# Kernel tuning notes

Measured on AMD Instinct MI355X. Metric: run time of the kernel, lower is better.

## Reference

```python
import jax, jax.numpy as jnp
import numpy as np

N_NODES = 50000
N_EDGES = 800000
IN_FEAT = 128
HID = 64
HEADS = 4
OUT = 40
NEG_SLOPE = 0.2


def _p(key, shape, scale=0.05):
    return jax.random.normal(key, shape, dtype=jnp.float32) * scale


def setup_inputs() -> dict:
    key = jax.random.key(0)
    ks = jax.random.split(key, 20)
    HW = HID * HEADS  # 256
    inp = {
        "x": jax.random.normal(ks[0], (N_NODES, IN_FEAT), dtype=jnp.float32),
        "edge_index": jax.random.randint(ks[1], (2, N_EDGES), 0, N_NODES, dtype=jnp.int64),
        # GATConv 1: in=128 -> heads=4, C=64
        "W1": _p(ks[2], (IN_FEAT, HW)), "as1": _p(ks[3], (HEADS, HID)), "ad1": _p(ks[4], (HEADS, HID)), "b1": jnp.zeros((HW,), jnp.float32),
        # GATConv 2: in=256
        "W2": _p(ks[5], (HW, HW)), "as2": _p(ks[6], (HEADS, HID)), "ad2": _p(ks[7], (HEADS, HID)), "b2": jnp.zeros((HW,), jnp.float32),
        # GATConv 3: in=256
        "W3": _p(ks[8], (HW, HW)), "as3": _p(ks[9], (HEADS, HID)), "ad3": _p(ks[10], (HEADS, HID)), "b3": jnp.zeros((HW,), jnp.float32),
        # MLP head: Linear(256,256) + Linear(256,40)
        "Wm1": _p(ks[11], (HW, HW)), "bm1": jnp.zeros((HW,), jnp.float32),
        "Wm2": _p(ks[12], (HW, OUT)), "bm2": jnp.zeros((OUT,), jnp.float32),
    }
    return inp


def gat_conv(x, src, dst, W, a_src, a_dst, bias, num_nodes):
    """PyG GATConv: concat=True, add_self_loops=True, leaky_relu(0.2)."""
    H, C = a_src.shape
    h = (x @ W).reshape(num_nodes, H, C)            # [N,H,C]
    # per-node attention logits (computed once, gathered per edge)
    src_logit = jnp.einsum('nhc,hc->nh', h, a_src)  # [N,H]
    dst_logit = jnp.einsum('nhc,hc->nh', h, a_dst)  # [N,H]
    # add self loops
    loop = jnp.arange(num_nodes, dtype=src.dtype)
    s = jnp.concatenate([src, loop])
    d = jnp.concatenate([dst, loop])
    alpha = jax.nn.leaky_relu(src_logit[s] + dst_logit[d], NEG_SLOPE)  # [E,H]
    # segment softmax over incoming edges of each destination node
    amax = jax.ops.segment_max(alpha, d, num_segments=num_nodes)
    e = jnp.exp(alpha - amax[d])
    denom = jax.ops.segment_sum(e, d, num_segments=num_nodes)
    coef = e / denom[d]                              # [E,H]
    msg = h[s] * coef[:, :, None]                    # [E,H,C] gather+weight
    out = jax.ops.segment_sum(msg, d, num_segments=num_nodes)  # [N,H,C]
    return out.reshape(num_nodes, H * C) + bias


def reference(x, edge_index, W1, as1, ad1, b1, W2, as2, ad2, b2, W3, as3, ad3, b3, Wm1, bm1, Wm2, bm2):
    src, dst = edge_index[0], edge_index[1]
    n = x.shape[0]
    h = jax.nn.relu(gat_conv(x, src, dst, W1, as1, ad1, b1, n))
    h = jax.nn.relu(gat_conv(h, src, dst, W2, as2, ad2, b2, n))
    h = jax.nn.relu(gat_conv(h, src, dst, W3, as3, ad3, b3, n))
    h = jax.nn.relu(h @ Wm1 + bm1)
    return h @ Wm2 + bm2
```

## Files before the change

kernel.cpp:

```cpp
#include <hip/hip_runtime.h>


constexpr int NN = 50000;
constexpr int NE = 800000;
constexpr int NN_PAD = 50176;
constexpr int CAP = 48;

typedef _Float16 f16x8 __attribute__((ext_vector_type(8)));
typedef _Float16 f16x4 __attribute__((ext_vector_type(4)));
typedef float    f32x4 __attribute__((ext_vector_type(4)));

__device__ __forceinline__ void cp16(void* lds, const void* g)
{
    __builtin_amdgcn_global_load_lds(
        (const __attribute__((address_space(1))) uint32_t*)g,
        (__attribute__((address_space(3))) uint32_t*)lds, 16, 0, 0);
}

__global__ __launch_bounds__(256)
void convert_all_kernel(const float* __restrict__ W1, const float* __restrict__ W2,
                        const float* __restrict__ W3, const float* __restrict__ Wm1,
                        const float* __restrict__ Wm2,
                        _Float16* B1h, _Float16* B1l, _Float16* B2h, _Float16* B2l,
                        _Float16* B3h, _Float16* B3l, _Float16* Bmh, _Float16* Bml,
                        _Float16* Whh, _Float16* Whl)
{
    int idx = blockIdx.x * 256 + (int)threadIdx.x;
    const float* W; _Float16 *H, *Lo; int K, local;
    if (idx < 32768)       { W = W1;  H = B1h; Lo = B1l; K = 128; local = idx; }
    else if (idx < 98304)  { W = W2;  H = B2h; Lo = B2l; K = 256; local = idx - 32768; }
    else if (idx < 163840) { W = W3;  H = B3h; Lo = B3l; K = 256; local = idx - 98304; }
    else if (idx < 229376) { W = Wm1; H = Bmh; Lo = Bml; K = 256; local = idx - 163840; }
    else if (idx < 241664) {
        int l = idx - 229376; int n = l >> 8, k = l & 255;
        float v = (n < 40) ? Wm2[k * 40 + n] : 0.f;
        _Float16 h = (_Float16)v;
        Whh[l] = h; Whl[l] = (_Float16)(v - (float)h);
        return;
    } else return;
    int k = local >> 8, n = local & 255;
    float v = W[local];
    _Float16 h = (_Float16)v;
    H[n * K + k] = h;
    Lo[n * K + k] = (_Float16)(v - (float)h);
}

template<bool FUSE, bool PRESPLIT, bool EMIT_SPLIT>
__global__ __launch_bounds__(512, 4)
void gemm_mfma(const float* __restrict__ A,
               const _Float16* Ah, const _Float16* Al,
               const _Float16* __restrict__ Bhi, const _Float16* __restrict__ Blo,
               const float* __restrict__ bias, float* __restrict__ C,
               _Float16* __restrict__ h16,
               _Float16* Oh, _Float16* Ol,
               const float* __restrict__ a_src, const float* __restrict__ a_dst,
               float* __restrict__ sl, float* __restrict__ dl,
               int M, int K)
{
    __shared__ __align__(16) _Float16 sAhi[128][32], sAlo[128][32];
    __shared__ __align__(16) _Float16 sBhi[256][32], sBlo[256][32];

    const int tid  = (int)threadIdx.x;
    const int wave = tid >> 6;
    const int mw   = wave >> 2;
    const int nw   = wave & 3;
    const int lane = tid & 63;
    const int l15  = lane & 15;
    const int quad = lane >> 4;
    const int swz  = (l15 >> 1) & 3;
    const int bm   = blockIdx.x * 128;

    f32x4 acc[4][4];
    #pragma unroll
    for (int i = 0; i < 4; ++i)
        #pragma unroll
        for (int j = 0; j < 4; ++j)
            acc[i][j] = (f32x4){0.f, 0.f, 0.f, 0.f};

    for (int k0 = 0; k0 < K; k0 += 32) {
        {
            int pos = lane & 3;
            #pragma unroll
            for (int j = 0; j < 2; ++j) {
                int rowB = wave * 32 + j * 16 + (lane >> 2);
                int c = pos ^ ((rowB >> 1) & 3);
                cp16(&sBhi[wave * 32 + j * 16][0], Bhi + (size_t)rowB * K + k0 + c * 8);
                cp16(&sBlo[wave * 32 + j * 16][0], Blo + (size_t)rowB * K + k0 + c * 8);
            }
        }
        if (PRESPLIT) {
            int pos = lane & 3;
            int rowA = wave * 16 + (lane >> 2);
            int c = pos ^ ((rowA >> 1) & 3);
            cp16(&sAhi[wave * 16][0], Ah + (size_t)(bm + rowA) * K + k0 + c * 8);
            cp16(&sAlo[wave * 16][0], Al + (size_t)(bm + rowA) * K + k0 + c * 8);
        } else {
            int r = tid >> 2, c = tid & 3;
            int grow = bm + r;
            float4 v0 = make_float4(0.f, 0.f, 0.f, 0.f), v1 = v0;
            if (grow < M) {
                v0 = *(const float4*)(A + (size_t)grow * K + k0 + c * 8);
                v1 = *(const float4*)(A + (size_t)grow * K + k0 + c * 8 + 4);
            }
            float fv[8] = {v0.x, v0.y, v0.z, v0.w, v1.x, v1.y, v1.z, v1.w};
            f16x8 h8, l8;
            #pragma unroll
            for (int u = 0; u < 8; ++u) {
                _Float16 hh = (_Float16)fv[u];
                h8[u] = hh; l8[u] = (_Float16)(fv[u] - (float)hh);
            }
            int slot = (c ^ ((r >> 1) & 3)) * 8;
            *(f16x8*)&sAhi[r][slot] = h8;
            *(f16x8*)&sAlo[r][slot] = l8;
        }
        __syncthreads();

        f16x8 bh[4], bl[4];
        #pragma unroll
        for (int nt = 0; nt < 4; ++nt) {
            int n = nw * 64 + nt * 16 + l15;
            bh[nt] = *(const f16x8*)&sBhi[n][(quad ^ swz) * 8];
            bl[nt] = *(const f16x8*)&sBlo[n][(quad ^ swz) * 8];
        }
        #pragma unroll
        for (int mt = 0; mt < 4; ++mt) {
            int m = mw * 64 + mt * 16 + l15;
            f16x8 ah = *(const f16x8*)&sAhi[m][(quad ^ swz) * 8];
            f16x8 al = *(const f16x8*)&sAlo[m][(quad ^ swz) * 8];
            #pragma unroll
            for (int nt = 0; nt < 4; ++nt) {
                acc[mt][nt] = __builtin_amdgcn_mfma_f32_16x16x32_f16(ah, bh[nt], acc[mt][nt], 0, 0, 0);
                acc[mt][nt] = __builtin_amdgcn_mfma_f32_16x16x32_f16(al, bh[nt], acc[mt][nt], 0, 0, 0);
                acc[mt][nt] = __builtin_amdgcn_mfma_f32_16x16x32_f16(ah, bl[nt], acc[mt][nt], 0, 0, 0);
            }
        }
        __syncthreads();
    }

    float aS[4], aD[4];
    if (FUSE) {
        #pragma unroll
        for (int nt = 0; nt < 4; ++nt) {
            aS[nt] = a_src[nw * 64 + nt * 16 + l15];
            aD[nt] = a_dst[nw * 64 + nt * 16 + l15];
        }
    }

    #pragma unroll
    for (int mt = 0; mt < 4; ++mt) {
        #pragma unroll
        for (int r = 0; r < 4; ++r) {
            int row = bm + mw * 64 + mt * 16 + quad * 4 + r;
            bool ok = (row < M);
            if (ok) {
                #pragma unroll
                for (int nt = 0; nt < 4; ++nt) {
                    int col = nw * 64 + nt * 16 + l15;
                    float c = acc[mt][nt][r];
                    if (EMIT_SPLIT) {
                        float v = fmaxf(c + bias[col], 0.f);
                        _Float16 hh = (_Float16)v;
                        Oh[(size_t)row * 256 + col] = hh;
                        Ol[(size_t)row * 256 + col] = (_Float16)(v - (float)hh);
                    } else {
                        C[(size_t)row * 256 + col] = c;
                        if (FUSE) h16[(size_t)row * 256 + col] = (_Float16)c;
                    }
                }
            }
            if (FUSE) {
                float vs = 0.f, vd = 0.f;
                #pragma unroll
                for (int nt = 0; nt < 4; ++nt) {
                    float c = acc[mt][nt][r];
                    vs = fmaf(c, aS[nt], vs);
                    vd = fmaf(c, aD[nt], vd);
                }
                #pragma unroll
                for (int off = 8; off >= 1; off >>= 1) {
                    vs += __shfl_xor(vs, off, 64);
                    vd += __shfl_xor(vd, off, 64);
                }
                if (l15 == 0 && ok) {
                    sl[row * 4 + nw] = vs;
                    dl[row * 4 + nw] = vd;
                }
            }
        }
    }
}

__global__ __launch_bounds__(256)
void gemm_head(const _Float16* __restrict__ Ah, const _Float16* __restrict__ Al,
               const _Float16* __restrict__ Bh, const _Float16* __restrict__ Bl,
               const float* __restrict__ bias, float* __restrict__ out, int M)
{
    __shared__ _Float16 sAhi[256][40], sAlo[256][40];
    __shared__ _Float16 sBhi[48][40],  sBlo[48][40];

    const int tid  = (int)threadIdx.x;
    const int wave = tid >> 6;
    const int lane = tid & 63;
    const int l15  = lane & 15;
    const int quad = lane >> 4;
    const int bm   = blockIdx.x * 256;

    f32x4 acc[4][3];
    #pragma unroll
    for (int i = 0; i < 4; ++i)
        #pragma unroll
        for (int j = 0; j < 3; ++j)
            acc[i][j] = (f32x4){0.f, 0.f, 0.f, 0.f};

    for (int k0 = 0; k0 < 256; k0 += 32) {
        #pragma unroll
        for (int i = 0; i < 4; ++i) {
            int idx = tid + i * 256;
            int row = idx >> 2, kq = (idx & 3) * 8;
            int grow = bm + row;
            uint4 vh = {0,0,0,0}, vl = {0,0,0,0};
            if (grow < M) {
                vh = *(const uint4*)(Ah + (size_t)grow * 256 + k0 + kq);
                vl = *(const uint4*)(Al + (size_t)grow * 256 + k0 + kq);
            }
            *(uint4*)&sAhi[row][kq] = vh;
            *(uint4*)&sAlo[row][kq] = vl;
        }
        if (tid < 192) {
            int n = tid >> 2, kq = (tid & 3) * 8;
            *(uint4*)&sBhi[n][kq] = *(const uint4*)(Bh + (size_t)n * 256 + k0 + kq);
            *(uint4*)&sBlo[n][kq] = *(const uint4*)(Bl + (size_t)n * 256 + k0 + kq);
        }
        __syncthreads();

        f16x8 bh[3], bl[3];
        #pragma unroll
        for (int nt = 0; nt < 3; ++nt) {
            int n = nt * 16 + l15;
            bh[nt] = *(const f16x8*)&sBhi[n][quad * 8];
            bl[nt] = *(const f16x8*)&sBlo[n][quad * 8];
        }
        #pragma unroll
        for (int mt = 0; mt < 4; ++mt) {
            int m = wave * 64 + mt * 16 + l15;
            f16x8 ah = *(const f16x8*)&sAhi[m][quad * 8];
            f16x8 al = *(const f16x8*)&sAlo[m][quad * 8];
            #pragma unroll
            for (int nt = 0; nt < 3; ++nt) {
                acc[mt][nt] = __builtin_amdgcn_mfma_f32_16x16x32_f16(ah, bh[nt], acc[mt][nt], 0, 0, 0);
                acc[mt][nt] = __builtin_amdgcn_mfma_f32_16x16x32_f16(al, bh[nt], acc[mt][nt], 0, 0, 0);
                acc[mt][nt] = __builtin_amdgcn_mfma_f32_16x16x32_f16(ah, bl[nt], acc[mt][nt], 0, 0, 0);
            }
        }
        __syncthreads();
    }

    #pragma unroll
    for (int mt = 0; mt < 4; ++mt) {
        #pragma unroll
        for (int r = 0; r < 4; ++r) {
            int row = bm + wave * 64 + mt * 16 + quad * 4 + r;
            if (row >= M) continue;
            #pragma unroll
            for (int nt = 0; nt < 3; ++nt) {
                int col = nt * 16 + l15;
                if (col < 40)
                    out[(size_t)row * 40 + col] = acc[mt][nt][r] + bias[col];
            }
        }
    }
}

__device__ __forceinline__ float leaky02(float a) {
    return (a >= 0.f) ? a : 0.2f * a;
}

__global__ __launch_bounds__(256)
void scatter_kernel(const int* __restrict__ src, const int* __restrict__ dst,
                    int* __restrict__ cursor, int* __restrict__ bucket)
{
    int e = blockIdx.x * 256 + (int)threadIdx.x;
    if (e >= NE) return;
    int d = dst[e];
    int pos = atomicAdd(&cursor[d], 1);
    if (pos < CAP) bucket[d * CAP + pos] = src[e];
}

__global__ __launch_bounds__(256)
void gat_aggregate(const int* __restrict__ cursor, const int* __restrict__ bucket,
                   const float* __restrict__ sl, const float* __restrict__ dl,
                   const float* __restrict__ hlin, const _Float16* __restrict__ h16,
                   const float* __restrict__ bias,
                   _Float16* __restrict__ Ph, _Float16* __restrict__ Pl)
{
    int n = blockIdx.x * 4 + ((int)threadIdx.x >> 6);
    if (n >= NN) return;
    const int lane = (int)threadIdx.x & 63;
    const int head = lane >> 4;
    const float dlh = dl[n * 4 + head];

    float exs = __expf(leaky02(sl[n * 4 + head] + dlh));
    float4 hn = *(const float4*)(hlin + (size_t)n * 256 + lane * 4);
    float4 a0; float d0 = exs;
    a0.x = exs * hn.x; a0.y = exs * hn.y; a0.z = exs * hn.z; a0.w = exs * hn.w;
    float4 a1 = {0,0,0,0}, a2 = {0,0,0,0}, a3 = {0,0,0,0};
    float d1 = 0.f, d2 = 0.f, d3 = 0.f;

    const int* bkt = bucket + (size_t)n * CAP;
    const int cnt = min(cursor[n], CAP);
    int i = 0;
    for (; i + 3 < cnt; i += 4) {
        int s0 = bkt[i], s1 = bkt[i + 1], s2 = bkt[i + 2], s3 = bkt[i + 3];
        float v0 = sl[s0 * 4 + head], v1 = sl[s1 * 4 + head];
        float v2 = sl[s2 * 4 + head], v3 = sl[s3 * 4 + head];
        f16x4 h0 = *(const f16x4*)(h16 + (size_t)s0 * 256 + lane * 4);
        f16x4 h1 = *(const f16x4*)(h16 + (size_t)s1 * 256 + lane * 4);
        f16x4 h2 = *(const f16x4*)(h16 + (size_t)s2 * 256 + lane * 4);
        f16x4 h3 = *(const f16x4*)(h16 + (size_t)s3 * 256 + lane * 4);
        float e0 = __expf(leaky02(v0 + dlh));
        float e1 = __expf(leaky02(v1 + dlh));
        float e2 = __expf(leaky02(v2 + dlh));
        float e3 = __expf(leaky02(v3 + dlh));
        a0.x = fmaf(e0, (float)h0[0], a0.x); a0.y = fmaf(e0, (float)h0[1], a0.y);
        a0.z = fmaf(e0, (float)h0[2], a0.z); a0.w = fmaf(e0, (float)h0[3], a0.w);
        d0 += e0;
        a1.x = fmaf(e1, (float)h1[0], a1.x); a1.y = fmaf(e1, (float)h1[1], a1.y);
        a1.z = fmaf(e1, (float)h1[2], a1.z); a1.w = fmaf(e1, (float)h1[3], a1.w);
        d1 += e1;
        a2.x = fmaf(e2, (float)h2[0], a2.x); a2.y = fmaf(e2, (float)h2[1], a2.y);
        a2.z = fmaf(e2, (float)h2[2], a2.z); a2.w = fmaf(e2, (float)h2[3], a2.w);
        d2 += e2;
        a3.x = fmaf(e3, (float)h3[0], a3.x); a3.y = fmaf(e3, (float)h3[1], a3.y);
        a3.z = fmaf(e3, (float)h3[2], a3.z); a3.w = fmaf(e3, (float)h3[3], a3.w);
        d3 += e3;
    }
    for (; i < cnt; ++i) {
        int s0 = bkt[i];
        float v0 = sl[s0 * 4 + head];
        f16x4 h0 = *(const f16x4*)(h16 + (size_t)s0 * 256 + lane * 4);
        float e0 = __expf(leaky02(v0 + dlh));
        a0.x = fmaf(e0, (float)h0[0], a0.x); a0.y = fmaf(e0, (float)h0[1], a0.y);
        a0.z = fmaf(e0, (float)h0[2], a0.z); a0.w = fmaf(e0, (float)h0[3], a0.w);
        d0 += e0;
    }
    float4 acc;
    acc.x = (a0.x + a1.x) + (a2.x + a3.x);
    acc.y = (a0.y + a1.y) + (a2.y + a3.y);
    acc.z = (a0.z + a1.z) + (a2.z + a3.z);
    acc.w = (a0.w + a1.w) + (a2.w + a3.w);
    float denom = (d0 + d1) + (d2 + d3);

    float inv = 1.f / denom;
    float4 bv = *(const float4*)(bias + lane * 4);
    float rv[4];
    rv[0] = fmaxf(bv.x + acc.x * inv, 0.f);
    rv[1] = fmaxf(bv.y + acc.y * inv, 0.f);
    rv[2] = fmaxf(bv.z + acc.z * inv, 0.f);
    rv[3] = fmaxf(bv.w + acc.w * inv, 0.f);
    f16x4 h, l;
    #pragma unroll
    for (int u = 0; u < 4; ++u) {
        _Float16 hh = (_Float16)rv[u];
        h[u] = hh; l[u] = (_Float16)(rv[u] - (float)hh);
    }
    *(f16x4*)(Ph + (size_t)n * 256 + lane * 4) = h;
    *(f16x4*)(Pl + (size_t)n * 256 + lane * 4) = l;
}

extern "C" void kernel_launch(void* const* d_in, const int* in_sizes, int n_in,
                              void* d_out, int out_size, void* d_ws, size_t ws_size,
                              hipStream_t stream)
{
    const float* x   = (const float*)d_in[0];
    const int*   ei  = (const int*)d_in[1];
    const int* src = ei;
    const int* dst = ei + NE;
    const float* W1  = (const float*)d_in[2];
    const float* as1 = (const float*)d_in[3];
    const float* ad1 = (const float*)d_in[4];
    const float* b1  = (const float*)d_in[5];
    const float* W2  = (const float*)d_in[6];
    const float* as2 = (const float*)d_in[7];
    const float* ad2 = (const float*)d_in[8];
    const float* b2  = (const float*)d_in[9];
    const float* W3  = (const float*)d_in[10];
    const float* as3 = (const float*)d_in[11];
    const float* ad3 = (const float*)d_in[12];
    const float* b3  = (const float*)d_in[13];
    const float* Wm1 = (const float*)d_in[14];
    const float* bm1 = (const float*)d_in[15];
    const float* Wm2 = (const float*)d_in[16];
    const float* bm2 = (const float*)d_in[17];
    float* out = (float*)d_out;

    float* ws  = (float*)d_ws;
    float* L   = ws;
    float* sl  = L + (size_t)NN * 256;
    float* dl  = sl + NN * 4;
    int* cursor = (int*)(dl + NN * 4);
    int* bucket = cursor + NN;
    uintptr_t fb = (uintptr_t)(bucket + (size_t)NN * CAP);
    fb = (fb + 15) & ~(uintptr_t)15;
    _Float16* wb = (_Float16*)fb;
    _Float16* B1h = wb;                 _Float16* B1l = B1h + 256 * 128;
    _Float16* B2h = B1l + 256 * 128;    _Float16* B2l = B2h + 256 * 256;
    _Float16* B3h = B2l + 256 * 256;    _Float16* B3l = B3h + 256 * 256;
    _Float16* Bmh = B3l + 256 * 256;    _Float16* Bml = Bmh + 256 * 256;
    _Float16* Whh = Bml + 256 * 256;    _Float16* Whl = Whh + 48 * 256;
    _Float16* H16 = Whl + 48 * 256;
    _Float16* Ph  = H16 + (size_t)NN * 256;
    _Float16* Pl  = Ph  + (size_t)NN_PAD * 256;

    const dim3 block(256);
    const dim3 block512(512);
    const dim3 mfmaGrid((NN + 127) / 128);
    const dim3 headGrid((NN + 255) / 256);
    const int neBlocks  = (NE + 255) / 256;
    const int nodeWaveBlocks = (NN + 3) / 4;

    convert_all_kernel<<<944, block, 0, stream>>>(
        W1, W2, W3, Wm1, Wm2, B1h, B1l, B2h, B2l, B3h, B3l, Bmh, Bml, Whh, Whl);
    (void)hipMemsetAsync(cursor, 0, (size_t)NN * sizeof(int), stream);
    scatter_kernel<<<neBlocks, block, 0, stream>>>(src, dst, cursor, bucket);

    gemm_mfma<true, false, false><<<mfmaGrid, block512, 0, stream>>>(
        x, nullptr, nullptr, B1h, B1l, nullptr, L, H16, nullptr, nullptr,
        as1, ad1, sl, dl, NN, 128);
    gat_aggregate<<<nodeWaveBlocks, block, 0, stream>>>(cursor, bucket, sl, dl, L, H16, b1, Ph, Pl);

    gemm_mfma<true, true, false><<<mfmaGrid, block512, 0, stream>>>(
        nullptr, Ph, Pl, B2h, B2l, nullptr, L, H16, nullptr, nullptr,
        as2, ad2, sl, dl, NN, 256);
    gat_aggregate<<<nodeWaveBlocks, block, 0, stream>>>(cursor, bucket, sl, dl, L, H16, b2, Ph, Pl);

    gemm_mfma<true, true, false><<<mfmaGrid, block512, 0, stream>>>(
        nullptr, Ph, Pl, B3h, B3l, nullptr, L, H16, nullptr, nullptr,
        as3, ad3, sl, dl, NN, 256);
    gat_aggregate<<<nodeWaveBlocks, block, 0, stream>>>(cursor, bucket, sl, dl, L, H16, b3, Ph, Pl);

    gemm_mfma<false, true, true><<<mfmaGrid, block512, 0, stream>>>(
        nullptr, Ph, Pl, Bmh, Bml, bm1, nullptr, nullptr, Ph, Pl,
        nullptr, nullptr, nullptr, nullptr, NN, 256);
    gemm_head<<<headGrid, block, 0, stream>>>(Ph, Pl, Whh, Whl, bm2, out, NN);
}
```

Measured before the change: 578.0 us.

## Pack two nodes per wave in aggregation and replace fp32 features with fp16 hi/lo split

The GEMM epilogue now stores the projected features as an fp16 hi/lo pair instead of an fp32 copy plus an fp16 copy, which cuts write traffic. The aggregation kernel now handles two destination nodes per wave, 32 lanes each, with 8-wide fp16 gathers per lane. It runs a predicated, unrolled neighbor loop bounded by the larger of the two nodes' degrees. The aim is wider gathers, more memory-level parallelism, and fewer bytes per GEMM epilogue. The cost is divergent wasted iterations when the paired nodes have different degrees, plus more registers per thread.

```diff
diff --git a/kernel.cpp b/kernel.cpp
--- a/kernel.cpp
+++ b/kernel.cpp
@@ -50,8 +50,8 @@
 void gemm_mfma(const float* __restrict__ A,
                const _Float16* Ah, const _Float16* Al,
                const _Float16* __restrict__ Bhi, const _Float16* __restrict__ Blo,
-               const float* __restrict__ bias, float* __restrict__ C,
-               _Float16* __restrict__ h16,
+               const float* __restrict__ bias,
+               _Float16* __restrict__ h16, _Float16* __restrict__ h16lo,
                _Float16* Oh, _Float16* Ol,
                const float* __restrict__ a_src, const float* __restrict__ a_dst,
                float* __restrict__ sl, float* __restrict__ dl,
@@ -163,8 +163,9 @@
                         Oh[(size_t)row * 256 + col] = hh;
                         Ol[(size_t)row * 256 + col] = (_Float16)(v - (float)hh);
                     } else {
-                        C[(size_t)row * 256 + col] = c;
-                        if (FUSE) h16[(size_t)row * 256 + col] = (_Float16)c;
+                        _Float16 hh = (_Float16)c;
+                        h16[(size_t)row * 256 + col] = hh;
+                        h16lo[(size_t)row * 256 + col] = (_Float16)(c - (float)hh);
                     }
                 }
             }
@@ -289,82 +290,69 @@
 __global__ __launch_bounds__(256)
 void gat_aggregate(const int* __restrict__ cursor, const int* __restrict__ bucket,
                    const float* __restrict__ sl, const float* __restrict__ dl,
-                   const float* __restrict__ hlin, const _Float16* __restrict__ h16,
+                   const _Float16* __restrict__ h16, const _Float16* __restrict__ h16lo,
                    const float* __restrict__ bias,
                    _Float16* __restrict__ Ph, _Float16* __restrict__ Pl)
 {
-    int n = blockIdx.x * 4 + ((int)threadIdx.x >> 6);
-    if (n >= NN) return;
-    const int lane = (int)threadIdx.x & 63;
-    const int head = lane >> 4;
+    const int tid  = (int)threadIdx.x;
+    const int wave = tid >> 6;
+    const int lane = tid & 63;
+    const int half = lane >> 5;
+    const int cl   = lane & 31;
+    const int head = cl >> 3;
+    const int n    = blockIdx.x * 8 + wave * 2 + half;
+
     const float dlh = dl[n * 4 + head];
 
     float exs = __expf(leaky02(sl[n * 4 + head] + dlh));
-    float4 hn = *(const float4*)(hlin + (size_t)n * 256 + lane * 4);
-    float4 a0; float d0 = exs;
-    a0.x = exs * hn.x; a0.y = exs * hn.y; a0.z = exs * hn.z; a0.w = exs * hn.w;
-    float4 a1 = {0,0,0,0}, a2 = {0,0,0,0}, a3 = {0,0,0,0};
-    float d1 = 0.f, d2 = 0.f, d3 = 0.f;
-
+    f16x8 shi = *(const f16x8*)(h16   + (size_t)n * 256 + cl * 8);
+    f16x8 slo = *(const f16x8*)(h16lo + (size_t)n * 256 + cl * 8);
+    float acc[4][8];
+    float den[4] = {exs, 0.f, 0.f, 0.f};
+    #pragma unroll
+    for (int k = 0; k < 8; ++k)
+        acc[0][k] = exs * ((float)shi[k] + (float)slo[k]);
+    #pragma unroll
+    for (int j = 1; j < 4; ++j)
+        #pragma unroll
+        for (int k = 0; k < 8; ++k) acc[j][k] = 0.f;
+
+    const int cnt = min(cursor[n], CAP);
+    const int maxc = max(cnt, __shfl_xor(cnt, 32, 64));
     const int* bkt = bucket + (size_t)n * CAP;
-    const int cnt = min(cursor[n], CAP);
-    int i = 0;
-    for (; i + 3 < cnt; i += 4) {
-        int s0 = bkt[i], s1 = bkt[i + 1], s2 = bkt[i + 2], s3 = bkt[i + 3];
-        float v0 = sl[s0 * 4 + head], v1 = sl[s1 * 4 + head];
-        float v2 = sl[s2 * 4 + head], v3 = sl[s3 * 4 + head];
-        f16x4 h0 = *(const f16x4*)(h16 + (size_t)s0 * 256 + lane * 4);
-        f16x4 h1 = *(const f16x4*)(h16 + (size_t)s1 * 256 + lane * 4);
-        f16x4 h2 = *(const f16x4*)(h16 + (size_t)s2 * 256 + lane * 4);
-        f16x4 h3 = *(const f16x4*)(h16 + (size_t)s3 * 256 + lane * 4);
-        float e0 = __expf(leaky02(v0 + dlh));
-        float e1 = __expf(leaky02(v1 + dlh));
-        float e2 = __expf(leaky02(v2 + dlh));
-        float e3 = __expf(leaky02(v3 + dlh));
-        a0.x = fmaf(e0, (float)h0[0], a0.x); a0.y = fmaf(e0, (float)h0[1], a0.y);
-        a0.z = fmaf(e0, (float)h0[2], a0.z); a0.w = fmaf(e0, (float)h0[3], a0.w);
-        d0 += e0;
-        a1.x = fmaf(e1, (float)h1[0], a1.x); a1.y = fmaf(e1, (float)h1[1], a1.y);
-        a1.z = fmaf(e1, (float)h1[2], a1.z); a1.w = fmaf(e1, (float)h1[3], a1.w);
-        d1 += e1;
-        a2.x = fmaf(e2, (float)h2[0], a2.x); a2.y = fmaf(e2, (float)h2[1], a2.y);
-        a2.z = fmaf(e2, (float)h2[2], a2.z); a2.w = fmaf(e2, (float)h2[3], a2.w);
-        d2 += e2;
-        a3.x = fmaf(e3, (float)h3[0], a3.x); a3.y = fmaf(e3, (float)h3[1], a3.y);
-        a3.z = fmaf(e3, (float)h3[2], a3.z); a3.w = fmaf(e3, (float)h3[3], a3.w);
-        d3 += e3;
-    }
-    for (; i < cnt; ++i) {
-        int s0 = bkt[i];
-        float v0 = sl[s0 * 4 + head];
-        f16x4 h0 = *(const f16x4*)(h16 + (size_t)s0 * 256 + lane * 4);
-        float e0 = __expf(leaky02(v0 + dlh));
-        a0.x = fmaf(e0, (float)h0[0], a0.x); a0.y = fmaf(e0, (float)h0[1], a0.y);
-        a0.z = fmaf(e0, (float)h0[2], a0.z); a0.w = fmaf(e0, (float)h0[3], a0.w);
-        d0 += e0;
-    }
-    float4 acc;
-    acc.x = (a0.x + a1.x) + (a2.x + a3.x);
-    acc.y = (a0.y + a1.y) + (a2.y + a3.y);
-    acc.z = (a0.z + a1.z) + (a2.z + a3.z);
-    acc.w = (a0.w + a1.w) + (a2.w + a3.w);
-    float denom = (d0 + d1) + (d2 + d3);
-
+
+    for (int base = 0; base < maxc; base += 4) {
+        #pragma unroll
+        for (int j = 0; j < 4; ++j) {
+            int idx = base + j;
+            bool v = idx < cnt;
+            int s = v ? bkt[idx] : 0;
+            float lv = sl[s * 4 + head];
+            f16x8 hv = *(const f16x8*)(h16 + (size_t)s * 256 + cl * 8);
+            float e = v ? __expf(leaky02(lv + dlh)) : 0.f;
+            #pragma unroll
+            for (int k = 0; k < 8; ++k)
+                acc[j][k] = fmaf(e, (float)hv[k], acc[j][k]);
+            den[j] += e;
+        }
+    }
+
+    float denom = (den[0] + den[1]) + (den[2] + den[3]);
     float inv = 1.f / denom;
-    float4 bv = *(const float4*)(bias + lane * 4);
-    float rv[4];
-    rv[0] = fmaxf(bv.x + acc.x * inv, 0.f);
-    rv[1] = fmaxf(bv.y + acc.y * inv, 0.f);
-    rv[2] = fmaxf(bv.z + acc.z * inv, 0.f);
-    rv[3] = fmaxf(bv.w + acc.w * inv, 0.f);
-    f16x4 h, l;
-    #pragma unroll
-    for (int u = 0; u < 4; ++u) {
-        _Float16 hh = (_Float16)rv[u];
-        h[u] = hh; l[u] = (_Float16)(rv[u] - (float)hh);
-    }
-    *(f16x4*)(Ph + (size_t)n * 256 + lane * 4) = h;
-    *(f16x4*)(Pl + (size_t)n * 256 + lane * 4) = l;
+    float4 b0 = *(const float4*)(bias + cl * 8);
+    float4 b1 = *(const float4*)(bias + cl * 8 + 4);
+    float bb[8] = {b0.x, b0.y, b0.z, b0.w, b1.x, b1.y, b1.z, b1.w};
+    f16x8 oh, ol;
+    #pragma unroll
+    for (int k = 0; k < 8; ++k) {
+        float a = (acc[0][k] + acc[1][k]) + (acc[2][k] + acc[3][k]);
+        float r = fmaxf(bb[k] + a * inv, 0.f);
+        _Float16 hh = (_Float16)r;
+        oh[k] = hh;
+        ol[k] = (_Float16)(r - (float)hh);
+    }
+    *(f16x8*)(Ph + (size_t)n * 256 + cl * 8) = oh;
+    *(f16x8*)(Pl + (size_t)n * 256 + cl * 8) = ol;
 }
 
 extern "C" void kernel_launch(void* const* d_in, const int* in_sizes, int n_in,
@@ -394,8 +382,7 @@
     float* out = (float*)d_out;
 
     float* ws  = (float*)d_ws;
-    float* L   = ws;
-    float* sl  = L + (size_t)NN * 256;
+    float* sl  = ws;
     float* dl  = sl + NN * 4;
     int* cursor = (int*)(dl + NN * 4);
     int* bucket = cursor + NN;
@@ -407,16 +394,17 @@
     _Float16* B3h = B2l + 256 * 256;    _Float16* B3l = B3h + 256 * 256;
     _Float16* Bmh = B3l + 256 * 256;    _Float16* Bml = Bmh + 256 * 256;
     _Float16* Whh = Bml + 256 * 256;    _Float16* Whl = Whh + 48 * 256;
-    _Float16* H16 = Whl + 48 * 256;
-    _Float16* Ph  = H16 + (size_t)NN * 256;
-    _Float16* Pl  = Ph  + (size_t)NN_PAD * 256;
+    _Float16* H16  = Whl + 48 * 256;
+    _Float16* H16l = H16 + (size_t)NN * 256;
+    _Float16* Ph  = H16l + (size_t)NN * 256;
+    _Float16* Pl  = Ph   + (size_t)NN_PAD * 256;
 
     const dim3 block(256);
     const dim3 block512(512);
     const dim3 mfmaGrid((NN + 127) / 128);
     const dim3 headGrid((NN + 255) / 256);
-    const int neBlocks  = (NE + 255) / 256;
-    const int nodeWaveBlocks = (NN + 3) / 4;
+    const int neBlocks = (NE + 255) / 256;
+    const int aggBlocks = NN / 8;
 
     convert_all_kernel<<<944, block, 0, stream>>>(
         W1, W2, W3, Wm1, Wm2, B1h, B1l, B2h, B2l, B3h, B3l, Bmh, Bml, Whh, Whl);
@@ -424,19 +412,19 @@
     scatter_kernel<<<neBlocks, block, 0, stream>>>(src, dst, cursor, bucket);
 
     gemm_mfma<true, false, false><<<mfmaGrid, block512, 0, stream>>>(
-        x, nullptr, nullptr, B1h, B1l, nullptr, L, H16, nullptr, nullptr,
+        x, nullptr, nullptr, B1h, B1l, nullptr, H16, H16l, nullptr, nullptr,
         as1, ad1, sl, dl, NN, 128);
-    gat_aggregate<<<nodeWaveBlocks, block, 0, stream>>>(cursor, bucket, sl, dl, L, H16, b1, Ph, Pl);
+    gat_aggregate<<<aggBlocks, block, 0, stream>>>(cursor, bucket, sl, dl, H16, H16l, b1, Ph, Pl);
 
     gemm_mfma<true, true, false><<<mfmaGrid, block512, 0, stream>>>(
-        nullptr, Ph, Pl, B2h, B2l, nullptr, L, H16, nullptr, nullptr,
+        nullptr, Ph, Pl, B2h, B2l, nullptr, H16, H16l, nullptr, nullptr,
         as2, ad2, sl, dl, NN, 256);
-    gat_aggregate<<<nodeWaveBlocks, block, 0, stream>>>(cursor, bucket, sl, dl, L, H16, b2, Ph, Pl);
+    gat_aggregate<<<aggBlocks, block, 0, stream>>>(cursor, bucket, sl, dl, H16, H16l, b2, Ph, Pl);
 
     gemm_mfma<true, true, false><<<mfmaGrid, block512, 0, stream>>>(
-        nullptr, Ph, Pl, B3h, B3l, nullptr, L, H16, nullptr, nullptr,
+        nullptr, Ph, Pl, B3h, B3l, nullptr, H16, H16l, nullptr, nullptr,
         as3, ad3, sl, dl, NN, 256);
-    gat_aggregate<<<nodeWaveBlocks, block, 0, stream>>>(cursor, bucket, sl, dl, L, H16, b3, Ph, Pl);
+    gat_aggregate<<<aggBlocks, block, 0, stream>>>(cursor, bucket, sl, dl, H16, H16l, b3, Ph, Pl);
 
     gemm_mfma<false, true, true><<<mfmaGrid, block512, 0, stream>>>(
         nullptr, Ph, Pl, Bmh, Bml, bm1, nullptr, nullptr, Ph, Pl,
```

Result: slower. 603.1 us (+4.3%).
